# Optimization experiments

Measured on AMD Instinct MI355X. Metric: run time of the kernel, lower is better.

Reference implementation:

```python
import jax, jax.numpy as jnp
import numpy as np

D = 128
HP = 32
WP = 32
M = 64
B = 8
T = 16
DECAY = 2.0
EPS = 1e-5


def _rope(x, h, w):
    # x: (..., D); h, w: integer coords broadcastable against x's leading dims.
    # Replicates the torch in-place update order: the 'second' channel of each
    # pair is rotated using the ALREADY-updated first channel.
    lead = x.shape[:-1]
    d = x.shape[-1]
    xg = x.reshape(lead + (d // 4, 4))
    # channel layout within group g: [4g (h-a), 4g+1 (w-a), 4g+2 (h-b), 4g+3 (w-b)]
    theta = 100.0 ** (-4.0 * jnp.arange(1, d // 4 + 1, dtype=x.dtype) / d)  # (d//4,)
    hf = h[..., None].astype(x.dtype)
    wf = w[..., None].astype(x.dtype)
    ch, sh = jnp.cos(theta * hf), jnp.sin(theta * hf)
    cw, sw = jnp.cos(theta * wf), jnp.sin(theta * wf)
    a, c, b, e = xg[..., 0], xg[..., 1], xg[..., 2], xg[..., 3]
    a2 = a * ch - b * sh
    b2 = b * ch - a2 * sh  # uses updated a2 (in-place semantics)
    c2 = c * cw + e * sw
    e2 = e * cw + c2 * sw  # uses updated c2
    return jnp.stack([a2, c2, b2, e2], axis=-1).reshape(lead + (d,))


def _layernorm(x, g, b):
    mu = jnp.mean(x, axis=-1, keepdims=True)
    var = jnp.mean((x - mu) ** 2, axis=-1, keepdims=True)
    return (x - mu) * jax.lax.rsqrt(var + EPS) * g + b


def setup_inputs() -> dict:
    key = jax.random.key(0)
    ks = jax.random.split(key, 6)
    t = jax.random.normal(ks[0], (B, T, M, D), dtype=jnp.float32)
    mv = jax.random.normal(ks[1], (B, T, HP, WP, D), dtype=jnp.float32)
    positions = jax.random.randint(ks[2], (B, T, M), 0, HP * WP, dtype=jnp.int64)
    Wq = jax.random.normal(ks[3], (D, D), dtype=jnp.float32) * 0.02
    Wk = jax.random.normal(ks[4], (D, D), dtype=jnp.float32) * 0.02
    return {
        "t": t, "mv": mv, "positions": positions,
        "Wq": Wq, "bq": jnp.zeros((D,), jnp.float32),
        "Wk": Wk, "bk": jnp.zeros((D,), jnp.float32),
        "ln_g": jnp.ones((D,), jnp.float32), "ln_b": jnp.zeros((D,), jnp.float32),
    }


def reference(t, mv, positions, Wq, bq, Wk, bk, ln_g, ln_b):
    Bb, Tt, Mm, Dd = t.shape
    _, _, H, W, _ = mv.shape
    P = H * W

    q = t @ Wq.T + bq                     # (B,T,M,D)
    k = mv @ Wk.T + bk                    # (B,T,H,W,D)

    gh, gw = jnp.meshgrid(jnp.arange(H), jnp.arange(W), indexing="ij")
    k = _rope(k, gh, gw)                  # square rope over the patch grid
    ph = positions // W
    pw = positions % W
    q = _rope(q, ph, pw)                  # flat rope at per-token positions

    q = _layernorm(q.reshape(Bb * Tt, Mm, Dd), ln_g, ln_b)
    k = _layernorm(k.reshape(Bb * Tt, P, Dd), ln_g, ln_b)

    att = jnp.einsum("bmd,bpd->bmp", q, k) / jnp.sqrt(jnp.float32(Dd))

    # distance bias
    pos_coords = jnp.stack([ph, pw], axis=-1).astype(jnp.float32)   # (B,T,M,2)
    p = jnp.arange(P)
    patch_coords = jnp.stack([p // W, p % W], axis=-1).astype(jnp.float32)  # (P,2)
    diff = pos_coords[..., None, :] - patch_coords                  # (B,T,M,P,2)
    dist = jnp.sqrt(jnp.sum(diff * diff, axis=-1))
    bias = -dist / (2.0 * DECAY ** 2)
    bias = jnp.where((pos_coords[..., 0] < 0)[..., None], -1e9, bias)
    bias = bias.reshape(Bb * Tt, Mm, P)

    att = jax.nn.softmax(att + bias, axis=-1)
    out = jnp.einsum("bmp,bpd->bmd", att, mv.reshape(Bb * Tt, P, Dd))
    return out.reshape(Bb, Tt, Mm, Dd)
```

## Files before the change

### kernel.cpp

```cpp
#include <hip/hip_runtime.h>
#include <math.h>

#define D   128
#define HP  32
#define WP  32
#define M   64
#define Bb  8
#define Tt  16
#define P   (HP*WP)
#define BT  (Bb*Tt)
#define EPSF 1e-5f
#define SCALE 0.08838834764831845f

typedef __attribute__((ext_vector_type(8))) _Float16 half8;
typedef __attribute__((ext_vector_type(8))) short    short8;
typedef __attribute__((ext_vector_type(4))) float    floatx4;

__global__ __launch_bounds__(1024)
void prep(const float* __restrict__ Wq, const float* __restrict__ Wk,
          _Float16* __restrict__ W16q, _Float16* __restrict__ W16k,
          float2* __restrict__ ropetab)
{
  const int b = blockIdx.x, t = threadIdx.x;
  if (b == 0) {
    const int gq = t >> 5, coord = t & 31;
    const float theta = __powf(100.0f, -4.0f*(float)(gq+1)/128.0f);
    float s, c;
    __sincosf(theta*(float)coord, &s, &c);
    ropetab[t] = make_float2(c, s);
  } else if (b <= 16) {
    const int i = (b-1)*1024 + t;
    W16q[i] = (_Float16)Wq[i];
  } else {
    const int i = (b-17)*1024 + t;
    W16k[i] = (_Float16)Wk[i];
  }
}

template<bool IS_Q>
__global__ __launch_bounds__(256)
void proj_reg(const float* __restrict__ xin,
              const _Float16* __restrict__ W16,
              const float* __restrict__ bvec,
              const float* __restrict__ g,
              const float* __restrict__ bln,
              const int*   __restrict__ positions,
              const float2* __restrict__ ropetab,
              _Float16* __restrict__ yout,
              _Float16* __restrict__ vt)
{
  const int tid = threadIdx.x;
  const int w = tid >> 6, lane = tid & 63;
  const int gg = lane >> 4, c = lane & 15;
  const int block0 = blockIdx.x * 64;

  __shared__ _Float16 wl[128*128];

  {
    const short8* wg = (const short8*)W16;
    #pragma unroll
    for (int it = 0; it < 8; ++it) {
      const int idx = tid + 256*it;
      const int row = idx >> 4, col8 = idx & 15;
      const short8 v = wg[idx];
      const int byte = row*256 + col8*16;
      *(short8*)((char*)wl + (byte ^ ((row&7)<<4))) = v;
    }
  }
  __syncthreads();

  const float* xr = xin + (size_t)(block0 + w*16 + c) * D;
  half8 aq[4];
  #pragma unroll
  for (int ks = 0; ks < 4; ++ks) {
    const float4 f0 = *(const float4*)(xr + ks*32 + gg*8);
    const float4 f1 = *(const float4*)(xr + ks*32 + gg*8 + 4);
    _Float16 h[8] = {(_Float16)f0.x,(_Float16)f0.y,(_Float16)f0.z,(_Float16)f0.w,
                     (_Float16)f1.x,(_Float16)f1.y,(_Float16)f1.z,(_Float16)f1.w};
    aq[ks] = *(half8*)h;
  }

  floatx4 acc[8];
  #pragma unroll
  for (int jt = 0; jt < 8; ++jt) {
    floatx4 a4 = (floatx4){0.f,0.f,0.f,0.f};
    #pragma unroll
    for (int ks = 0; ks < 4; ++ks) {
      const int brow = jt*16 + c;
      const int byte = brow*256 + (gg*8 + ks*32)*2;
      const half8 bf = *(const half8*)((const char*)wl + (byte ^ ((brow&7)<<4)));
      a4 = __builtin_amdgcn_mfma_f32_16x16x32_f16(aq[ks], bf, a4, 0, 0, 0);
    }
    acc[jt] = a4;
  }

  if constexpr (!IS_Q) {
    __syncthreads();
    _Float16* xs = wl;
    {
      const float4* xg = (const float4*)(xin + (size_t)block0 * D);
      #pragma unroll
      for (int it = 0; it < 4; ++it) {
        const int idx = tid + 256*it;
        const int row = idx >> 4, col8 = idx & 15;
        const float4 f0 = xg[idx*2], f1 = xg[idx*2+1];
        _Float16 h[8] = {(_Float16)f0.x,(_Float16)f0.y,(_Float16)f0.z,(_Float16)f0.w,
                         (_Float16)f1.x,(_Float16)f1.y,(_Float16)f1.z,(_Float16)f1.w};
        const int byte = row*256 + col8*16;
        *(half8*)((char*)xs + (byte ^ ((row&7)<<4))) = *(half8*)h;
      }
    }
    __syncthreads();
    {
      const int bt2 = block0 >> 10;
      const int p0  = block0 & (P-1);
      const int dd  = tid & 127, ph2 = tid >> 7;
      short hv[32];
      #pragma unroll
      for (int i = 0; i < 32; ++i) {
        const int pl2 = ph2*32 + i;
        const int byte = pl2*256 + dd*2;
        hv[i] = *(const short*)((const char*)xs + (byte ^ ((pl2&7)<<4)));
      }
      short8* dst = (short8*)(vt + ((size_t)bt2*D + dd)*P + p0 + ph2*32);
      #pragma unroll
      for (int i = 0; i < 4; ++i) dst[i] = ((short8*)hv)[i];
    }
  }

  const int rr = c & 3;
  int coordv[4];
  #pragma unroll
  for (int r = 0; r < 4; ++r) {
    const int grow = block0 + w*16 + gg*4 + r;
    int hh, ww;
    if (IS_Q) { const int pos = positions[grow]; hh = pos >> 5; ww = pos & 31; }
    else      { const int p = grow & (P-1);      hh = p  >> 5; ww = p  & 31; }
    coordv[r] = (rr & 1) ? ww : hh;
  }

  float fin[8][4];
  float s1[4] = {0.f,0.f,0.f,0.f}, s2[4] = {0.f,0.f,0.f,0.f};
  #pragma unroll
  for (int jt = 0; jt < 8; ++jt) {
    const float bj = bvec[jt*16 + c];
    const int gq = jt*4 + (c >> 2);
    #pragma unroll
    for (int r = 0; r < 4; ++r) {
      const float val = acc[jt][r] + bj;
      const float2 tt = ropetab[gq*32 + coordv[r]];
      const float p2 = __shfl_xor(val, 2);
      const float f1v = (rr & 1) ? (val*tt.x + p2*tt.y)
                                 : (val*tt.x - p2*tt.y);
      const float g2 = __shfl_xor(f1v, 2);
      const float fn = (rr >= 2)
          ? ((rr & 1) ? (val*tt.x + g2*tt.y) : (val*tt.x - g2*tt.y))
          : f1v;
      fin[jt][r] = fn;
      s1[r] += fn;
      s2[r] += fn*fn;
    }
  }

  #pragma unroll
  for (int r = 0; r < 4; ++r) {
    #pragma unroll
    for (int off = 1; off <= 8; off <<= 1) {
      s1[r] += __shfl_xor(s1[r], off);
      s2[r] += __shfl_xor(s2[r], off);
    }
  }

  #pragma unroll
  for (int r = 0; r < 4; ++r) {
    const float mu   = s1[r] * (1.f/128.f);
    const float var  = s2[r] * (1.f/128.f) - mu*mu;
    const float rinv = rsqrtf(var + EPSF);
    const int grow = block0 + w*16 + gg*4 + r;
    _Float16* yo = yout + (size_t)grow * D;
    #pragma unroll
    for (int jt = 0; jt < 8; ++jt) {
      const int col = jt*16 + c;
      const float nv = (fin[jt][r] - mu) * rinv * g[col] + bln[col];
      yo[col] = (_Float16)nv;
    }
  }
}

__global__ __launch_bounds__(256)
void attn_mfma(const _Float16* __restrict__ q,
               const _Float16* __restrict__ k,
               const _Float16* __restrict__ vt,
               const int* __restrict__ positions,
               float* __restrict__ out)
{
  const int bt  = blockIdx.x & (BT-1);
  const int qq  = blockIdx.x >> 7;
  const int tid = threadIdx.x;
  const int w   = tid >> 6, lane = tid & 63;
  const int g   = lane >> 4, c = lane & 15;

  __shared__ _Float16 smem_h[4*16*136];
  __shared__ float    l_lds[4][16];
  _Float16 (*pl)[16][88]   = reinterpret_cast<_Float16(*)[16][88]>(smem_h);
  _Float16 (*o16)[16][136] = reinterpret_cast<_Float16(*)[16][136]>(smem_h);

  const _Float16* qrow = q + (size_t)(bt*M + qq*16 + c) * D + g*8;
  half8 aq[4];
  #pragma unroll
  for (int ks = 0; ks < 4; ++ks) aq[ks] = *(const half8*)(qrow + ks*32);

  float ph[4], pw[4];
  #pragma unroll
  for (int r = 0; r < 4; ++r) {
    const int pos = positions[bt*M + qq*16 + g*4 + r];
    ph[r] = (float)(pos >> 5); pw[r] = (float)(pos & 31);
  }

  float lsum[4] = {0.f, 0.f, 0.f, 0.f};
  floatx4 oacc[8];
  #pragma unroll
  for (int dt = 0; dt < 8; ++dt) oacc[dt] = (floatx4){0.f,0.f,0.f,0.f};

  const _Float16* kb = k  + ((size_t)bt * P) * D;
  const _Float16* vb = vt + ((size_t)bt * D) * P;

  for (int t = 0; t < 4; ++t) {
    const int p0 = w*256 + t*64;

    floatx4 s[4];
    #pragma unroll
    for (int pt = 0; pt < 4; ++pt) {
      floatx4 a4 = (floatx4){0.f,0.f,0.f,0.f};
      const _Float16* krow = kb + (size_t)(p0 + pt*16 + c) * D + g*8;
      #pragma unroll
      for (int ks = 0; ks < 4; ++ks)
        a4 = __builtin_amdgcn_mfma_f32_16x16x32_f16(
                 aq[ks], *(const half8*)(krow + ks*32), a4, 0, 0, 0);
      s[pt] = a4;
    }

    #pragma unroll
    for (int pt = 0; pt < 4; ++pt) {
      const int pp = p0 + pt*16 + c;
      const float hh = (float)(pp >> 5), ww = (float)(pp & 31);
      #pragma unroll
      for (int r = 0; r < 4; ++r) {
        const float dx = ph[r] - hh, dy = pw[r] - ww;
        const float sv = s[pt][r]*SCALE - 0.125f*sqrtf(dx*dx + dy*dy);
        const float e  = __expf(sv - 4.0f);
        const _Float16 eh = (_Float16)e;
        pl[w][g*4 + r][pt*16 + c] = eh;
        lsum[r] += (float)eh;
      }
    }

    #pragma unroll
    for (int ks = 0; ks < 2; ++ks) {
      const half8 pa = *(const half8*)(&pl[w][c][ks*32 + g*8]);
      #pragma unroll
      for (int dt = 0; dt < 8; ++dt) {
        const half8 bv = *(const half8*)(vb + (size_t)(dt*16 + c)*P
                                            + p0 + ks*32 + g*8);
        oacc[dt] = __builtin_amdgcn_mfma_f32_16x16x32_f16(pa, bv, oacc[dt], 0,0,0);
      }
    }
  }

  #pragma unroll
  for (int r = 0; r < 4; ++r) {
    #pragma unroll
    for (int off = 1; off <= 8; off <<= 1)
      lsum[r] += __shfl_xor(lsum[r], off);
  }
  if (c == 0) {
    #pragma unroll
    for (int r = 0; r < 4; ++r) l_lds[w][g*4 + r] = lsum[r];
  }

  #pragma unroll
  for (int dt = 0; dt < 8; ++dt)
    #pragma unroll
    for (int r = 0; r < 4; ++r)
      o16[w][g*4 + r][dt*16 + c] = (_Float16)oacc[dt][r];
  __syncthreads();

  const int qi = tid >> 4, dg = tid & 15;
  const float L = l_lds[0][qi] + l_lds[1][qi] + l_lds[2][qi] + l_lds[3][qi];
  const float inv = 1.0f / L;
  float a2[8] = {0.f,0.f,0.f,0.f,0.f,0.f,0.f,0.f};
  #pragma unroll
  for (int w2 = 0; w2 < 4; ++w2) {
    const half8 ov = *(const half8*)(&o16[w2][qi][dg*8]);
    #pragma unroll
    for (int dd = 0; dd < 8; ++dd) a2[dd] += (float)ov[dd];
  }
  float* orow = out + (size_t)(bt*M + qq*16 + qi) * D + dg*8;
  #pragma unroll
  for (int dd = 0; dd < 8; ++dd) orow[dd] = a2[dd] * inv;
}

extern "C" void kernel_launch(void* const* d_in, const int* in_sizes, int n_in,
                              void* d_out, int out_size, void* d_ws, size_t ws_size,
                              hipStream_t stream) {
  const float* t    = (const float*)d_in[0];
  const float* mv   = (const float*)d_in[1];
  const int*   pos  = (const int*)  d_in[2];
  const float* Wq   = (const float*)d_in[3];
  const float* bq   = (const float*)d_in[4];
  const float* Wk   = (const float*)d_in[5];
  const float* bk   = (const float*)d_in[6];
  const float* ln_g = (const float*)d_in[7];
  const float* ln_b = (const float*)d_in[8];
  float* out = (float*)d_out;

  _Float16* qbuf = (_Float16*)d_ws;
  _Float16* kbuf = qbuf + (size_t)BT*M*D;
  _Float16* vtbf = kbuf + (size_t)BT*P*D;
  _Float16* w16q = vtbf + (size_t)BT*P*D;
  _Float16* w16k = w16q + D*D;
  float2*   rtab = (float2*)(w16k + D*D);

  prep<<<33, 1024, 0, stream>>>(Wq, Wk, w16q, w16k, rtab);
  proj_reg<false><<<BT*P/64, 256, 0, stream>>>(mv, w16k, bk, ln_g, ln_b, nullptr,
                                               rtab, kbuf, vtbf);
  proj_reg<true ><<<BT*M/64, 256, 0, stream>>>(t,  w16q, bq, ln_g, ln_b, pos,
                                               rtab, qbuf, nullptr);
  attn_mfma<<<512, 256, 0, stream>>>(qbuf, kbuf, vtbf, pos, out);
}
```

Before: 91.92 us.

## Process 128 rows per K-projection block to amortize weight staging

The K projection kernel now handles 128 patch rows per block instead of 64, calling a shared 64-row GEMM helper twice. The 32 KB fp16 weight tile is therefore loaded into LDS once per 128 rows, and the grid is halved. The V transpose also covers 128 rows per block. In attention, the aliased P and O LDS buffers are split into separate arrays with an added barrier, which raises LDS use and may lower occupancy.

Measured after the change: 133.5 us. 1.45x slower.

```diff
diff --git a/kernel.cpp b/kernel.cpp
--- a/kernel.cpp
+++ b/kernel.cpp
@@ -38,36 +38,19 @@
 }
 
 template<bool IS_Q>
-__global__ __launch_bounds__(256)
-void proj_reg(const float* __restrict__ xin,
-              const _Float16* __restrict__ W16,
-              const float* __restrict__ bvec,
-              const float* __restrict__ g,
-              const float* __restrict__ bln,
-              const int*   __restrict__ positions,
-              const float2* __restrict__ ropetab,
-              _Float16* __restrict__ yout,
-              _Float16* __restrict__ vt)
+__device__ __forceinline__
+void gemm64(const float* __restrict__ xin,
+            const float* __restrict__ bvec,
+            const float* __restrict__ g,
+            const float* __restrict__ bln,
+            const int*   __restrict__ positions,
+            const float2* __restrict__ ropetab,
+            _Float16* __restrict__ yout,
+            const _Float16* wl, int block0)
 {
   const int tid = threadIdx.x;
   const int w = tid >> 6, lane = tid & 63;
   const int gg = lane >> 4, c = lane & 15;
-  const int block0 = blockIdx.x * 64;
-
-  __shared__ _Float16 wl[128*128];
-
-  {
-    const short8* wg = (const short8*)W16;
-    #pragma unroll
-    for (int it = 0; it < 8; ++it) {
-      const int idx = tid + 256*it;
-      const int row = idx >> 4, col8 = idx & 15;
-      const short8 v = wg[idx];
-      const int byte = row*256 + col8*16;
-      *(short8*)((char*)wl + (byte ^ ((row&7)<<4))) = v;
-    }
-  }
-  __syncthreads();
 
   const float* xr = xin + (size_t)(block0 + w*16 + c) * D;
   half8 aq[4];
@@ -92,40 +75,6 @@
       a4 = __builtin_amdgcn_mfma_f32_16x16x32_f16(aq[ks], bf, a4, 0, 0, 0);
     }
     acc[jt] = a4;
-  }
-
-  if constexpr (!IS_Q) {
-    __syncthreads();
-    _Float16* xs = wl;
-    {
-      const float4* xg = (const float4*)(xin + (size_t)block0 * D);
-      #pragma unroll
-      for (int it = 0; it < 4; ++it) {
-        const int idx = tid + 256*it;
-        const int row = idx >> 4, col8 = idx & 15;
-        const float4 f0 = xg[idx*2], f1 = xg[idx*2+1];
-        _Float16 h[8] = {(_Float16)f0.x,(_Float16)f0.y,(_Float16)f0.z,(_Float16)f0.w,
-                         (_Float16)f1.x,(_Float16)f1.y,(_Float16)f1.z,(_Float16)f1.w};
-        const int byte = row*256 + col8*16;
-        *(half8*)((char*)xs + (byte ^ ((row&7)<<4))) = *(half8*)h;
-      }
-    }
-    __syncthreads();
-    {
-      const int bt2 = block0 >> 10;
-      const int p0  = block0 & (P-1);
-      const int dd  = tid & 127, ph2 = tid >> 7;
-      short hv[32];
-      #pragma unroll
-      for (int i = 0; i < 32; ++i) {
-        const int pl2 = ph2*32 + i;
-        const int byte = pl2*256 + dd*2;
-        hv[i] = *(const short*)((const char*)xs + (byte ^ ((pl2&7)<<4)));
-      }
-      short8* dst = (short8*)(vt + ((size_t)bt2*D + dd)*P + p0 + ph2*32);
-      #pragma unroll
-      for (int i = 0; i < 4; ++i) dst[i] = ((short8*)hv)[i];
-    }
   }
 
   const int rr = c & 3;
@@ -188,6 +137,101 @@
 }
 
 __global__ __launch_bounds__(256)
+void proj_k128(const float* __restrict__ mv,
+               const _Float16* __restrict__ w16k,
+               const float* __restrict__ bk,
+               const float* __restrict__ g,
+               const float* __restrict__ bln,
+               const float2* __restrict__ ropetab,
+               _Float16* __restrict__ kout,
+               _Float16* __restrict__ vt)
+{
+  const int tid = threadIdx.x;
+  const int block0 = blockIdx.x * 128;
+
+  __shared__ _Float16 wl[128*128];
+
+  {
+    const short8* wg = (const short8*)w16k;
+    #pragma unroll
+    for (int it = 0; it < 8; ++it) {
+      const int idx = tid + 256*it;
+      const int row = idx >> 4, col8 = idx & 15;
+      const short8 v = wg[idx];
+      const int byte = row*256 + col8*16;
+      *(short8*)((char*)wl + (byte ^ ((row&7)<<4))) = v;
+    }
+  }
+  __syncthreads();
+
+  gemm64<false>(mv, bk, g, bln, nullptr, ropetab, kout, wl, block0);
+  gemm64<false>(mv, bk, g, bln, nullptr, ropetab, kout, wl, block0 + 64);
+
+  __syncthreads();
+
+  {
+    const float4* xg = (const float4*)(mv + (size_t)block0 * D);
+    #pragma unroll
+    for (int it = 0; it < 8; ++it) {
+      const int idx = tid + 256*it;
+      const int row = idx >> 4, col8 = idx & 15;
+      const float4 f0 = xg[idx*2], f1 = xg[idx*2+1];
+      _Float16 h[8] = {(_Float16)f0.x,(_Float16)f0.y,(_Float16)f0.z,(_Float16)f0.w,
+                       (_Float16)f1.x,(_Float16)f1.y,(_Float16)f1.z,(_Float16)f1.w};
+      const int byte = row*256 + col8*16;
+      *(half8*)((char*)wl + (byte ^ ((row&7)<<4))) = *(half8*)h;
+    }
+  }
+  __syncthreads();
+
+  {
+    const int bt2 = block0 >> 10;
+    const int p0  = block0 & (P-1);
+    const int d   = tid & 127, ph = tid >> 7;
+    #pragma unroll
+    for (int seg = 0; seg < 2; ++seg) {
+      short hv[32];
+      #pragma unroll
+      for (int i = 0; i < 32; ++i) {
+        const int pl2 = ph*64 + seg*32 + i;
+        const int byte = pl2*256 + d*2;
+        hv[i] = *(const short*)((const char*)wl + (byte ^ ((pl2&7)<<4)));
+      }
+      short8* dst = (short8*)(vt + ((size_t)bt2*D + d)*P + p0 + ph*64 + seg*32);
+      #pragma unroll
+      for (int i = 0; i < 4; ++i) dst[i] = ((short8*)hv)[i];
+    }
+  }
+}
+
+__global__ __launch_bounds__(256)
+void proj_q(const float* __restrict__ t,
+            const _Float16* __restrict__ w16q,
+            const float* __restrict__ bq,
+            const float* __restrict__ g,
+            const float* __restrict__ bln,
+            const int*   __restrict__ positions,
+            const float2* __restrict__ ropetab,
+            _Float16* __restrict__ qout)
+{
+  const int tid = threadIdx.x;
+  __shared__ _Float16 wl[128*128];
+  {
+    const short8* wg = (const short8*)w16q;
+    #pragma unroll
+    for (int it = 0; it < 8; ++it) {
+      const int idx = tid + 256*it;
+      const int row = idx >> 4, col8 = idx & 15;
+      const short8 v = wg[idx];
+      const int byte = row*256 + col8*16;
+      *(short8*)((char*)wl + (byte ^ ((row&7)<<4))) = v;
+    }
+  }
+  __syncthreads();
+  gemm64<true>(t, bq, g, bln, positions, ropetab, qout, wl, blockIdx.x * 64);
+}
+
+__global__ __launch_bounds__(256)
 void attn_mfma(const _Float16* __restrict__ q,
                const _Float16* __restrict__ k,
                const _Float16* __restrict__ vt,
@@ -200,10 +244,9 @@
   const int w   = tid >> 6, lane = tid & 63;
   const int g   = lane >> 4, c = lane & 15;
 
-  __shared__ _Float16 smem_h[4*16*136];
+  __shared__ _Float16 pl[4][16][88];
+  __shared__ _Float16 o16[4][16][136];
   __shared__ float    l_lds[4][16];
-  _Float16 (*pl)[16][88]   = reinterpret_cast<_Float16(*)[16][88]>(smem_h);
-  _Float16 (*o16)[16][136] = reinterpret_cast<_Float16(*)[16][136]>(smem_h);
 
   const _Float16* qrow = q + (size_t)(bt*M + qq*16 + c) * D + g*8;
   half8 aq[4];
@@ -266,6 +309,8 @@
       }
     }
   }
+
+  __syncthreads();
 
   #pragma unroll
   for (int r = 0; r < 4; ++r) {
@@ -322,9 +367,8 @@
   float2*   rtab = (float2*)(w16k + D*D);
 
   prep<<<33, 1024, 0, stream>>>(Wq, Wk, w16q, w16k, rtab);
-  proj_reg<false><<<BT*P/64, 256, 0, stream>>>(mv, w16k, bk, ln_g, ln_b, nullptr,
-                                               rtab, kbuf, vtbf);
-  proj_reg<true ><<<BT*M/64, 256, 0, stream>>>(t,  w16q, bq, ln_g, ln_b, pos,
-                                               rtab, qbuf, nullptr);
+  proj_k128<<<BT*P/128, 256, 0, stream>>>(mv, w16k, bk, ln_g, ln_b,
+                                          rtab, kbuf, vtbf);
+  proj_q<<<BT*M/64, 256, 0, stream>>>(t, w16q, bq, ln_g, ln_b, pos, rtab, qbuf);
   attn_mfma<<<512, 256, 0, stream>>>(qbuf, kbuf, vtbf, pos, out);
 }
```
